# Kernel optimization log

Measured on AMD Instinct MI355X. Metric: run time of the kernel, lower is better.

Reference implementation:

```python
import jax, jax.numpy as jnp
import numpy as np

B, S, D, H, W = 2, 2048, 1024, 16, 256
HD = D // H

def setup_inputs() -> dict:
    key = jax.random.key(0)
    k1, k2, k3 = jax.random.split(key, 3)
    x = jax.random.normal(k1, (B, S, D), dtype=jnp.float32)
    w_qkv = jax.random.normal(k2, (D, 3 * D), dtype=jnp.float32) * (D ** -0.5)
    b_qkv = jnp.zeros((3 * D,), dtype=jnp.float32)
    w_out = jax.random.normal(k3, (D, D), dtype=jnp.float32) * (D ** -0.5)
    b_out = jnp.zeros((D,), dtype=jnp.float32)
    return {"x": x, "w_qkv": w_qkv, "b_qkv": b_qkv, "w_out": w_out, "b_out": b_out}

def reference(x, w_qkv, b_qkv, w_out, b_out):
    b, s, d = x.shape
    qkv = x @ w_qkv + b_qkv                       # [B,S,3D]
    qkv = qkv.reshape(b, s, 3, H, HD)
    q = jnp.transpose(qkv[:, :, 0], (0, 2, 1, 3))  # [B,H,S,HD]
    k = jnp.transpose(qkv[:, :, 1], (0, 2, 1, 3))
    v = jnp.transpose(qkv[:, :, 2], (0, 2, 1, 3))
    # NOTE: original scales by d_model**0.5, not head_dim**0.5
    scores = jnp.einsum('bhqd,bhkd->bhqk', q, k) / (d ** 0.5)
    idx = jnp.arange(s)
    band = jnp.abs(idx[:, None] - idx[None, :]) <= W  # |i-j| <= window_size
    scores = jnp.where(band[None, None], scores, -jnp.inf)
    attn = jax.nn.softmax(scores, axis=-1)
    out = jnp.einsum('bhqk,bhkd->bhqd', attn, v)
    out = jnp.transpose(out, (0, 2, 1, 3)).reshape(b, s, d)
    return out @ w_out + b_out
```

## Files before the change

kernel.cpp:

```cpp
#include <hip/hip_runtime.h>
#include <cstdint>
#include <cmath>

typedef unsigned short u16;
typedef __attribute__((ext_vector_type(8))) short bf16x8;
typedef __attribute__((ext_vector_type(4))) float f32x4;
typedef __attribute__((ext_vector_type(8))) unsigned short u16x8;

#define DEV static __device__ __forceinline__

DEV u16 f2bf(float f) {
  union { float f; uint32_t u; } v; v.f = f;
  uint32_t r = (v.u + 0x7fffu + ((v.u >> 16) & 1u)) >> 16;
  return (u16)r;
}

DEV float fexp2(float x) { return exp2f(x); }

DEV void async16(void* lds, const void* g) {
  __builtin_amdgcn_global_load_lds(
      (const __attribute__((address_space(1))) uint32_t*)g,
      (__attribute__((address_space(3))) uint32_t*)lds, 16, 0, 0);
}

#define QSCALE 0.04508422002778011f

__global__ void conv8(const float* __restrict__ in, u16* __restrict__ out, int n8) {
  int i = blockIdx.x * 256 + threadIdx.x;
  if (i >= n8) return;
  const float4* p = (const float4*)in + (size_t)i * 2;
  float4 a = p[0], b = p[1];
  u16x8 ov;
  ov[0] = f2bf(a.x); ov[1] = f2bf(a.y); ov[2] = f2bf(a.z); ov[3] = f2bf(a.w);
  ov[4] = f2bf(b.x); ov[5] = f2bf(b.y); ov[6] = f2bf(b.z); ov[7] = f2bf(b.w);
  *(u16x8*)(out + (size_t)i * 8) = ov;
}

__global__ void tconv(const float* __restrict__ in, u16* __restrict__ out, int R, int Cdim) {
  __shared__ float t[32][33];
  const int tx = threadIdx.x & 31, ty = threadIdx.x >> 5;
  const int r0 = blockIdx.y * 32, c0 = blockIdx.x * 32;
#pragma unroll
  for (int k = 0; k < 4; ++k) {
    int r = ty + k * 8;
    t[r][tx] = in[(size_t)(r0 + r) * Cdim + c0 + tx];
  }
  __syncthreads();
#pragma unroll
  for (int k = 0; k < 4; ++k) {
    int cc = ty + k * 8;
    out[(size_t)(c0 + cc) * R + r0 + tx] = f2bf(t[tx][cc]);
  }
}

template <int EPI>
__global__ __launch_bounds__(256, 2) void gemm_bt(
    const u16* __restrict__ A, const u16* __restrict__ BT,
    const float* __restrict__ bias, float* __restrict__ C,
    u16* __restrict__ qb, u16* __restrict__ kbuf, u16* __restrict__ vtb,
    int Mdim, int Ndim, int Kdim)
{
  __shared__ u16 Alds[128 * 64];
  __shared__ u16 Blds[128 * 64];
  const int tid = threadIdx.x;
  const int wid = tid >> 6, lane = tid & 63;
  const int g = lane >> 4, c = lane & 15;
  const int wr = wid >> 1, wc = wid & 1;
  const int gx = gridDim.x;
  const int nwg = gx * gridDim.y;
  const int lin = blockIdx.y * gx + blockIdx.x;
  const int work = (lin & 7) * (nwg >> 3) + (lin >> 3);
  const int row0 = (work / gx) * 128, col0 = (work % gx) * 128;

  f32x4 acc[4][4] = {};

  for (int kt = 0; kt < Kdim; kt += 64) {
    __syncthreads();
#pragma unroll
    for (int it = 0; it < 4; ++it) {
      int chunk = wid * 256 + it * 64 + lane;
      int r = chunk >> 3, j = chunk & 7;
      int js = j ^ (r & 7);
      async16((char*)Alds + (wid * 256 + it * 64) * 16,
              A + (size_t)(row0 + r) * Kdim + kt + js * 8);
      async16((char*)Blds + (wid * 256 + it * 64) * 16,
              BT + (size_t)(col0 + r) * Kdim + kt + js * 8);
    }
    __syncthreads();
#pragma unroll
    for (int kk = 0; kk < 2; ++kk) {
      bf16x8 av[4], bv[4];
#pragma unroll
      for (int mi = 0; mi < 4; ++mi) {
        int r = wr * 64 + mi * 16 + c;
        int js = (kk * 4 + g) ^ (r & 7);
        av[mi] = *(const bf16x8*)((const char*)Alds + r * 128 + js * 16);
      }
#pragma unroll
      for (int ni = 0; ni < 4; ++ni) {
        int r = wc * 64 + ni * 16 + c;
        int js = (kk * 4 + g) ^ (r & 7);
        bv[ni] = *(const bf16x8*)((const char*)Blds + r * 128 + js * 16);
      }
#pragma unroll
      for (int mi = 0; mi < 4; ++mi)
#pragma unroll
        for (int ni = 0; ni < 4; ++ni)
          acc[mi][ni] = __builtin_amdgcn_mfma_f32_16x16x32_bf16(
              av[mi], bv[ni], acc[mi][ni], 0, 0, 0);
    }
  }

#pragma unroll
  for (int mi = 0; mi < 4; ++mi) {
#pragma unroll
    for (int ni = 0; ni < 4; ++ni) {
      int colg = col0 + wc * 64 + ni * 16 + c;
      float bsv = bias[colg];
#pragma unroll
      for (int r = 0; r < 4; ++r) {
        int rowg = row0 + wr * 64 + mi * 16 + g * 4 + r;
        float val = acc[mi][ni][r] + bsv;
        if (EPI == 0) {
          C[(size_t)rowg * Ndim + colg] = val;
        } else {
          int t = colg >> 10, rem = colg & 1023;
          int h = rem >> 6, hd = rem & 63;
          int b = rowg >> 11, s = rowg & 2047;
          size_t bho = (size_t)(b * 16 + h);
          if (t == 0)      qb  [(bho * 2048 + s) * 64 + hd] = f2bf(val * QSCALE);
          else if (t == 1) kbuf[(bho * 2048 + s) * 64 + hd] = f2bf(val);
          else             vtb [(bho * 64 + hd) * 2048 + s] = f2bf(val);
        }
      }
    }
  }
}

__global__ __launch_bounds__(512, 4) void attn_win(
    const u16* __restrict__ qb, const u16* __restrict__ kb,
    const u16* __restrict__ vtb, u16* __restrict__ hb)
{
  constexpr int S = 2048, W = 256;
  __shared__ u16 Klds[2][64 * 64];
  __shared__ u16 Vlds[2][64 * 64];
  __shared__ u16 Plds[8][16 * 64];

  const int tid = threadIdx.x, wid = tid >> 6, lane = tid & 63;
  const int g = lane >> 4, c = lane & 15;
  const int lin = blockIdx.x;
  const int work = (lin & 7) * 64 + (lin >> 3);
  const int qt = work & 15, bh = work >> 4;
  const int q0 = qt * 128;
  const int qr0 = q0 + wid * 16;
  const int qw = qr0 + c;
  const size_t bho = (size_t)bh * S * 64;

  bf16x8 aq[2];
  {
    const u16* qrow = qb + bho + (size_t)qw * 64;
    aq[0] = *(const bf16x8*)(qrow + g * 8);
    aq[1] = *(const bf16x8*)(qrow + 32 + g * 8);
  }
  f32x4 o[4] = {};
  float m = -1e30f, lsum = 0.f;

  const int kstart = (q0 - W > 0) ? (q0 - W) : 0;
  const int kend = (q0 + 128 + W < S) ? (q0 + 128 + W) : S;

  const int sr = tid >> 3, sj = tid & 7;
  const int sjs = sj ^ (sr & 7);
#define STAGE(buf, k0s)                                                         \
  {                                                                             \
    async16((char*)&Klds[buf][0] + tid * 16,                                    \
            kb + bho + (size_t)((k0s) + sr) * 64 + sjs * 8);                    \
    async16((char*)&Vlds[buf][0] + tid * 16,                                    \
            vtb + bho + (size_t)sr * S + (k0s) + sjs * 8);                      \
  }

  STAGE(0, kstart);
  asm volatile("s_waitcnt vmcnt(0)" ::: "memory");
  __syncthreads();

  int cur = 0;
  for (int k0 = kstart; k0 < kend; k0 += 64) {
    if (k0 + 64 < kend) STAGE(cur ^ 1, k0 + 64);

    const bool wave_active = !(k0 > qr0 + 15 + W) && !(k0 + 63 < qr0 - W);
    if (wave_active) {
      const u16* Kb = &Klds[cur][0];
      const u16* Vb = &Vlds[cur][0];

      f32x4 sacc[4] = {};
      __builtin_amdgcn_s_setprio(1);
#pragma unroll
      for (int kb4 = 0; kb4 < 4; ++kb4) {
        int krow = kb4 * 16 + c;
#pragma unroll
        for (int kk = 0; kk < 2; ++kk) {
          int js = (kk * 4 + g) ^ (krow & 7);
          bf16x8 bk = *(const bf16x8*)((const char*)Kb + krow * 128 + js * 16);
          sacc[kb4] = __builtin_amdgcn_mfma_f32_16x16x32_bf16(bk, aq[kk], sacc[kb4], 0, 0, 0);
        }
      }
      __builtin_amdgcn_s_setprio(0);

      const bool full = (k0 >= qr0 + 15 - W) && (k0 + 63 <= qr0 + W);
      float sl[4][4];
      if (full) {
#pragma unroll
        for (int kb4 = 0; kb4 < 4; ++kb4)
#pragma unroll
          for (int r = 0; r < 4; ++r) sl[kb4][r] = sacc[kb4][r];
      } else {
#pragma unroll
        for (int kb4 = 0; kb4 < 4; ++kb4) {
#pragma unroll
          for (int r = 0; r < 4; ++r) {
            int key = k0 + kb4 * 16 + g * 4 + r;
            int d = qw - key;
            bool valid = (d <= W) && (d >= -W);
            sl[kb4][r] = valid ? sacc[kb4][r] : -1e30f;
          }
        }
      }

      float mx = fmaxf(
          fmaxf(fmaxf(fmaxf(sl[0][0], sl[0][1]), fmaxf(sl[0][2], sl[0][3])),
                fmaxf(fmaxf(sl[1][0], sl[1][1]), fmaxf(sl[1][2], sl[1][3]))),
          fmaxf(fmaxf(fmaxf(sl[2][0], sl[2][1]), fmaxf(sl[2][2], sl[2][3])),
                fmaxf(fmaxf(sl[3][0], sl[3][1]), fmaxf(sl[3][2], sl[3][3]))));
      mx = fmaxf(mx, __shfl_xor(mx, 16));
      mx = fmaxf(mx, __shfl_xor(mx, 32));

      if (!__all(mx - m <= 8.0f)) {
        float mnew = fmaxf(m, mx);
        float fs = fexp2(m - mnew);
        m = mnew;
        lsum *= fs;
        float fsr[4];
#pragma unroll
        for (int r = 0; r < 4; ++r)
          fsr[r] = __shfl(fs, (lane & 48) | (((lane & 48) >> 2) + r));
#pragma unroll
        for (int nb = 0; nb < 4; ++nb)
#pragma unroll
          for (int r = 0; r < 4; ++r) o[nb][r] *= fsr[r];
      }

      float rsum = 0.f;
      u16* Pw = &Plds[wid][0];
#pragma unroll
      for (int kb4 = 0; kb4 < 4; ++kb4) {
        float p0, p1, p2, p3;
        if (full) {
          p0 = fexp2(sl[kb4][0] - m); p1 = fexp2(sl[kb4][1] - m);
          p2 = fexp2(sl[kb4][2] - m); p3 = fexp2(sl[kb4][3] - m);
        } else {
          p0 = (sl[kb4][0] > -1e29f) ? fexp2(sl[kb4][0] - m) : 0.f;
          p1 = (sl[kb4][1] > -1e29f) ? fexp2(sl[kb4][1] - m) : 0.f;
          p2 = (sl[kb4][2] > -1e29f) ? fexp2(sl[kb4][2] - m) : 0.f;
          p3 = (sl[kb4][3] > -1e29f) ? fexp2(sl[kb4][3] - m) : 0.f;
        }
        rsum += (p0 + p1) + (p2 + p3);
        uint32_t lo, hi;
        asm("v_cvt_pk_bf16_f32 %0, %1, %2" : "=v"(lo) : "v"(p0), "v"(p1));
        asm("v_cvt_pk_bf16_f32 %0, %1, %2" : "=v"(hi) : "v"(p2), "v"(p3));
        uint2 wv; wv.x = lo; wv.y = hi;
        *(uint2*)((char*)Pw + c * 128 + (((kb4 * 2 + (g >> 1)) ^ (c & 7)) << 4) +
                  ((g & 1) << 3)) = wv;
      }
      rsum += __shfl_xor(rsum, 16);
      rsum += __shfl_xor(rsum, 32);
      lsum += rsum;

      asm volatile("s_waitcnt lgkmcnt(0)" ::: "memory");
      __builtin_amdgcn_sched_barrier(0);
      __builtin_amdgcn_s_setprio(1);
#pragma unroll
      for (int ks = 0; ks < 2; ++ks) {
        int js = (ks * 4 + g) ^ (c & 7);
        bf16x8 pa = *(const bf16x8*)((const char*)Pw + c * 128 + js * 16);
#pragma unroll
        for (int nb = 0; nb < 4; ++nb) {
          int hd = nb * 16 + c;
          int vjs = (ks * 4 + g) ^ (hd & 7);
          bf16x8 bv = *(const bf16x8*)((const char*)Vb + hd * 128 + vjs * 16);
          o[nb] = __builtin_amdgcn_mfma_f32_16x16x32_bf16(pa, bv, o[nb], 0, 0, 0);
        }
      }
      __builtin_amdgcn_s_setprio(0);
    }

    asm volatile("s_waitcnt vmcnt(0)" ::: "memory");
    __syncthreads();
    cur ^= 1;
  }
#undef STAGE

  const int b = bh >> 4, h = bh & 15;
  float linv[4];
#pragma unroll
  for (int r = 0; r < 4; ++r)
    linv[r] = 1.0f / __shfl(lsum, (lane & 48) | (((lane & 48) >> 2) + r));
#pragma unroll
  for (int r = 0; r < 4; ++r) {
    int qr = qr0 + g * 4 + r;
#pragma unroll
    for (int nb = 0; nb < 4; ++nb) {
      int col = h * 64 + nb * 16 + c;
      hb[(size_t)(b * 2048 + qr) * 1024 + col] = f2bf(o[nb][r] * linv[r]);
    }
  }
}

extern "C" void kernel_launch(void* const* d_in, const int* in_sizes, int n_in,
                              void* d_out, int out_size, void* d_ws, size_t ws_size,
                              hipStream_t stream) {
  const float* x     = (const float*)d_in[0];
  const float* w_qkv = (const float*)d_in[1];
  const float* b_qkv = (const float*)d_in[2];
  const float* w_out = (const float*)d_in[3];
  const float* b_out = (const float*)d_in[4];
  float* out = (float*)d_out;

  char* ws = (char*)d_ws;
  const size_t MB = 1024 * 1024;
  u16* xbf   = (u16*)(ws);
  u16* wqT   = (u16*)(ws + 8 * MB);
  u16* woT   = (u16*)(ws + 14 * MB);
  u16* qbuf  = (u16*)(ws + 16 * MB);
  u16* kbuf  = (u16*)(ws + 24 * MB);
  u16* vtbuf = (u16*)(ws + 32 * MB);
  u16* hbuf  = (u16*)(ws + 40 * MB);

  conv8<<<dim3(4096 * 1024 / 8 / 256), 256, 0, stream>>>(x, xbf, 4096 * 1024 / 8);
  tconv<<<dim3(3072 / 32, 1024 / 32), 256, 0, stream>>>(w_qkv, wqT, 1024, 3072);
  tconv<<<dim3(1024 / 32, 1024 / 32), 256, 0, stream>>>(w_out, woT, 1024, 1024);
  gemm_bt<1><<<dim3(3072 / 128, 4096 / 128), 256, 0, stream>>>(
      xbf, wqT, b_qkv, nullptr, qbuf, kbuf, vtbuf, 4096, 3072, 1024);
  attn_win<<<dim3(512), 512, 0, stream>>>(qbuf, kbuf, vtbuf, hbuf);
  gemm_bt<0><<<dim3(1024 / 128, 4096 / 128), 256, 0, stream>>>(
      hbuf, woT, b_out, out, nullptr, nullptr, nullptr, 4096, 1024, 1024);
}
```

Before: 169.5 us.

## Add 256x256-tile QKV GEMM kernel with ping-pong LDS pipeline

Swaps the generic 128x128 QKV projection GEMM for a dedicated 256x256-tile kernel with 512 threads. It double-buffers A and B halves in LDS through async global-to-LDS loads, using XOR-swizzled layout and hand-placed waitcnt/barrier/setprio scheduling. The larger tile raises data reuse per byte loaded, and the interleaved staging is meant to overlap memory traffic with MFMA work. The cost is 192 blocks (fewer than the CU count), higher register and LDS pressure, and fragile manual vmcnt accounting.

New measurement: 193.8 us. +14.3%, slower.

```diff
diff --git a/kernel.cpp b/kernel.cpp
--- a/kernel.cpp
+++ b/kernel.cpp
@@ -137,6 +137,150 @@
   }
 }
 
+__global__ __launch_bounds__(512, 2) void gemm256_qkv(
+    const u16* __restrict__ A, const u16* __restrict__ BT,
+    const float* __restrict__ bias,
+    u16* __restrict__ qb, u16* __restrict__ kbuf, u16* __restrict__ vtb)
+{
+  constexpr int K = 1024, NIT = 8;
+  __shared__ u16 lds[2 * 2 * 2 * 8192];
+  const int tid = threadIdx.x;
+  const int lane = tid & 63, wid = tid >> 6;
+  const int g = lane >> 4, c = lane & 15;
+  const int wm = wid >> 2, wn = wid & 3;
+  const int lin = blockIdx.x;
+  const int work = (lin & 7) * 24 + (lin >> 3);
+  const int row0 = (work / 12) * 256, col0 = (work % 12) * 256;
+
+  const int ch0 = tid, ch1 = 512 + tid;
+  const int r0c = ch0 >> 3, j0 = (ch0 & 7) ^ (r0c & 7);
+  const int r1c = ch1 >> 3, j1 = (ch1 & 7) ^ (r1c & 7);
+
+#define STG(ab, buf, half, t)                                                     \
+  {                                                                               \
+    const u16* gp = (ab) ? BT : A;                                                \
+    const int gb = (ab) ? col0 : row0;                                            \
+    u16* lb = lds + (((buf) * 2 + (ab)) * 2 + (half)) * 8192;                     \
+    async16(lb + ch0 * 8, gp + (size_t)(gb + (half) * 128 + r0c) * K + (t) * 64 + j0 * 8); \
+    async16(lb + ch1 * 8, gp + (size_t)(gb + (half) * 128 + r1c) * K + (t) * 64 + j1 * 8); \
+  }
+#define LDA(buf, mh)                                                              \
+  {                                                                               \
+    const u16* rb = lds + (((buf) * 2 + 0) * 2 + (mh)) * 8192;                    \
+    _Pragma("unroll") for (int i = 0; i < 4; ++i) {                               \
+      int rr = wm * 64 + i * 16 + c;                                              \
+      _Pragma("unroll") for (int kk = 0; kk < 2; ++kk)                            \
+        aA[i][kk] = *(const bf16x8*)((const char*)rb + rr * 128 +                 \
+                                     (((kk * 4 + g) ^ (rr & 7)) * 16));           \
+    }                                                                             \
+  }
+#define LDB(buf, nh, dst)                                                         \
+  {                                                                               \
+    const u16* rb = lds + (((buf) * 2 + 1) * 2 + (wn >> 1)) * 8192;               \
+    _Pragma("unroll") for (int j = 0; j < 2; ++j) {                               \
+      int rr = (wn & 1) * 64 + (nh) * 32 + j * 16 + c;                            \
+      _Pragma("unroll") for (int kk = 0; kk < 2; ++kk)                            \
+        dst[j][kk] = *(const bf16x8*)((const char*)rb + rr * 128 +                \
+                                      (((kk * 4 + g) ^ (rr & 7)) * 16));          \
+    }                                                                             \
+  }
+#define MMA(mo, no, bsrc)                                                         \
+  __builtin_amdgcn_s_setprio(1);                                                  \
+  _Pragma("unroll") for (int i = 0; i < 4; ++i)                                   \
+    _Pragma("unroll") for (int j = 0; j < 2; ++j) {                               \
+      acc[(mo) + i][(no) + j] = __builtin_amdgcn_mfma_f32_16x16x32_bf16(          \
+          aA[i][0], bsrc[j][0], acc[(mo) + i][(no) + j], 0, 0, 0);                \
+      acc[(mo) + i][(no) + j] = __builtin_amdgcn_mfma_f32_16x16x32_bf16(          \
+          aA[i][1], bsrc[j][1], acc[(mo) + i][(no) + j], 0, 0, 0);                \
+    }                                                                             \
+  __builtin_amdgcn_s_setprio(0);                                                  \
+  __builtin_amdgcn_sched_barrier(0);
+#define BAR() __builtin_amdgcn_s_barrier()
+
+  f32x4 acc[8][4] = {};
+  bf16x8 aA[4][2], bB0[2][2], bB1[2][2];
+
+  STG(0, 0, 0, 0); STG(1, 0, 0, 0); STG(1, 0, 1, 0); STG(0, 0, 1, 0);
+  STG(0, 1, 0, 1); STG(1, 1, 0, 1); STG(1, 1, 1, 1);
+  asm volatile("s_waitcnt vmcnt(6)" ::: "memory");
+  BAR();
+
+  for (int it = 0; it < NIT; ++it) {
+    const int t1 = 2 * it + 1, t2 = 2 * it + 2, t3 = 2 * it + 3;
+    const bool pf = (it < NIT - 1);
+    LDA(0, 0); LDB(0, 0, bB0);
+    STG(0, 1, 1, t1);
+    BAR();
+    MMA(0, 0, bB0);
+    BAR();
+    LDB(0, 1, bB1);
+    if (pf) STG(0, 0, 0, t2);
+    BAR();
+    MMA(0, 2, bB1);
+    BAR();
+    LDA(0, 1);
+    if (pf) STG(1, 0, 0, t2);
+    BAR();
+    MMA(4, 0, bB0);
+    BAR();
+    if (pf) STG(1, 0, 1, t2);
+    BAR();
+    MMA(4, 2, bB1);
+    if (pf) { asm volatile("s_waitcnt vmcnt(8)" ::: "memory"); }
+    else    { asm volatile("s_waitcnt vmcnt(2)" ::: "memory"); }
+    BAR();
+    LDA(1, 0); LDB(1, 0, bB0);
+    if (pf) STG(0, 0, 1, t2);
+    BAR();
+    MMA(0, 0, bB0);
+    BAR();
+    LDB(1, 1, bB1);
+    if (pf) STG(0, 1, 0, t3);
+    BAR();
+    MMA(0, 2, bB1);
+    if (pf) { asm volatile("s_waitcnt vmcnt(10)" ::: "memory"); }
+    else    { asm volatile("s_waitcnt vmcnt(0)" ::: "memory"); }
+    BAR();
+    LDA(1, 1);
+    if (pf) STG(1, 1, 0, t3);
+    BAR();
+    MMA(4, 0, bB0);
+    BAR();
+    if (pf) STG(1, 1, 1, t3);
+    BAR();
+    MMA(4, 2, bB1);
+    if (pf) { asm volatile("s_waitcnt vmcnt(6)" ::: "memory"); }
+    BAR();
+  }
+#undef STG
+#undef LDA
+#undef LDB
+#undef MMA
+#undef BAR
+
+#pragma unroll
+  for (int MF = 0; MF < 8; ++MF) {
+#pragma unroll
+    for (int NF = 0; NF < 4; ++NF) {
+      int colg = col0 + wn * 64 + NF * 16 + c;
+      float bsv = bias[colg];
+      int rowb = row0 + (MF >> 2) * 128 + wm * 64 + (MF & 3) * 16 + g * 4;
+#pragma unroll
+      for (int r = 0; r < 4; ++r) {
+        int rowg = rowb + r;
+        float val = acc[MF][NF][r] + bsv;
+        int t = colg >> 10, rem = colg & 1023;
+        int h = rem >> 6, hd = rem & 63;
+        int b = rowg >> 11, s = rowg & 2047;
+        size_t bho = (size_t)(b * 16 + h);
+        if (t == 0)      qb  [(bho * 2048 + s) * 64 + hd] = f2bf(val * QSCALE);
+        else if (t == 1) kbuf[(bho * 2048 + s) * 64 + hd] = f2bf(val);
+        else             vtb [(bho * 64 + hd) * 2048 + s] = f2bf(val);
+      }
+    }
+  }
+}
+
 __global__ __launch_bounds__(512, 4) void attn_win(
     const u16* __restrict__ qb, const u16* __restrict__ kb,
     const u16* __restrict__ vtb, u16* __restrict__ hb)
@@ -337,8 +481,7 @@
   conv8<<<dim3(4096 * 1024 / 8 / 256), 256, 0, stream>>>(x, xbf, 4096 * 1024 / 8);
   tconv<<<dim3(3072 / 32, 1024 / 32), 256, 0, stream>>>(w_qkv, wqT, 1024, 3072);
   tconv<<<dim3(1024 / 32, 1024 / 32), 256, 0, stream>>>(w_out, woT, 1024, 1024);
-  gemm_bt<1><<<dim3(3072 / 128, 4096 / 128), 256, 0, stream>>>(
-      xbf, wqT, b_qkv, nullptr, qbuf, kbuf, vtbuf, 4096, 3072, 1024);
+  gemm256_qkv<<<dim3(192), 512, 0, stream>>>(xbf, wqT, b_qkv, qbuf, kbuf, vtbuf);
   attn_win<<<dim3(512), 512, 0, stream>>>(qbuf, kbuf, vtbuf, hbuf);
   gemm_bt<0><<<dim3(1024 / 128, 4096 / 128), 256, 0, stream>>>(
       hbuf, woT, b_out, out, nullptr, nullptr, nullptr, 4096, 1024, 1024);
```

## Triple-buffer K/V tiles in windowed attention and vectorize V-transpose epilogue stores

Applied to the files above, without the earlier changes.

The attention kernel moves from double to triple buffering of K/V LDS tiles. It issues loads two tiles ahead and waits with a partial vmcnt, so each iteration needs one barrier instead of a full drain plus syncthreads. The QKV GEMM epilogue now packs four consecutive sequence positions into one 8-byte store for the transposed V buffer, and folds the Q/K paths into a single loop. LDS use per block grows by two 8KB tiles, which could lower occupancy under the 4-blocks-per-CU launch bound.

Result: faster. 161.9 us (-4.5%).

```diff
diff --git a/kernel.cpp b/kernel.cpp
--- a/kernel.cpp
+++ b/kernel.cpp
@@ -6,6 +6,7 @@
 typedef __attribute__((ext_vector_type(8))) short bf16x8;
 typedef __attribute__((ext_vector_type(4))) float f32x4;
 typedef __attribute__((ext_vector_type(8))) unsigned short u16x8;
+typedef __attribute__((ext_vector_type(4))) unsigned short u16x4;
 
 #define DEV static __device__ __forceinline__
 
@@ -117,20 +118,27 @@
     for (int ni = 0; ni < 4; ++ni) {
       int colg = col0 + wc * 64 + ni * 16 + c;
       float bsv = bias[colg];
-#pragma unroll
-      for (int r = 0; r < 4; ++r) {
-        int rowg = row0 + wr * 64 + mi * 16 + g * 4 + r;
-        float val = acc[mi][ni][r] + bsv;
-        if (EPI == 0) {
-          C[(size_t)rowg * Ndim + colg] = val;
+      int rowb = row0 + wr * 64 + mi * 16 + g * 4;
+      if (EPI == 0) {
+#pragma unroll
+        for (int r = 0; r < 4; ++r)
+          C[(size_t)(rowb + r) * Ndim + colg] = acc[mi][ni][r] + bsv;
+      } else {
+        int t = colg >> 10, rem = colg & 1023;
+        int h = rem >> 6, hd = rem & 63;
+        int b = rowb >> 11, s0 = rowb & 2047;
+        size_t bho = (size_t)(b * 16 + h);
+        if (t == 2) {
+          u16x4 pv;
+#pragma unroll
+          for (int r = 0; r < 4; ++r) pv[r] = f2bf(acc[mi][ni][r] + bsv);
+          *(u16x4*)(vtb + (bho * 64 + hd) * 2048 + s0) = pv;
         } else {
-          int t = colg >> 10, rem = colg & 1023;
-          int h = rem >> 6, hd = rem & 63;
-          int b = rowg >> 11, s = rowg & 2047;
-          size_t bho = (size_t)(b * 16 + h);
-          if (t == 0)      qb  [(bho * 2048 + s) * 64 + hd] = f2bf(val * QSCALE);
-          else if (t == 1) kbuf[(bho * 2048 + s) * 64 + hd] = f2bf(val);
-          else             vtb [(bho * 64 + hd) * 2048 + s] = f2bf(val);
+          u16* dst = (t == 0) ? qb : kbuf;
+          float sc = (t == 0) ? QSCALE : 1.0f;
+#pragma unroll
+          for (int r = 0; r < 4; ++r)
+            dst[(bho * 2048 + (s0 + r)) * 64 + hd] = f2bf((acc[mi][ni][r] + bsv) * sc);
         }
       }
     }
@@ -142,8 +150,8 @@
     const u16* __restrict__ vtb, u16* __restrict__ hb)
 {
   constexpr int S = 2048, W = 256;
-  __shared__ u16 Klds[2][64 * 64];
-  __shared__ u16 Vlds[2][64 * 64];
+  __shared__ u16 Klds[3][64 * 64];
+  __shared__ u16 Vlds[3][64 * 64];
   __shared__ u16 Plds[8][16 * 64];
 
   const int tid = threadIdx.x, wid = tid >> 6, lane = tid & 63;
@@ -167,6 +175,7 @@
 
   const int kstart = (q0 - W > 0) ? (q0 - W) : 0;
   const int kend = (q0 + 128 + W < S) ? (q0 + 128 + W) : S;
+  const int ntiles = (kend - kstart) >> 6;
 
   const int sr = tid >> 3, sj = tid & 7;
   const int sjs = sj ^ (sr & 7);
@@ -179,13 +188,17 @@
   }
 
   STAGE(0, kstart);
-  asm volatile("s_waitcnt vmcnt(0)" ::: "memory");
-  __syncthreads();
-
-  int cur = 0;
-  for (int k0 = kstart; k0 < kend; k0 += 64) {
-    if (k0 + 64 < kend) STAGE(cur ^ 1, k0 + 64);
-
+  if (ntiles > 1) STAGE(1, kstart + 64);
+
+  for (int i = 0; i < ntiles; ++i) {
+    const int k0 = kstart + (i << 6);
+    if (i + 1 < ntiles) { asm volatile("s_waitcnt vmcnt(2)" ::: "memory"); }
+    else                { asm volatile("s_waitcnt vmcnt(0)" ::: "memory"); }
+    __builtin_amdgcn_s_barrier();
+    __builtin_amdgcn_sched_barrier(0);
+    if (i + 2 < ntiles) STAGE((i + 2) % 3, k0 + 128);
+
+    const int cur = i % 3;
     const bool wave_active = !(k0 > qr0 + 15 + W) && !(k0 + 63 < qr0 - W);
     if (wave_active) {
       const u16* Kb = &Klds[cur][0];
@@ -291,10 +304,6 @@
       }
       __builtin_amdgcn_s_setprio(0);
     }
-
-    asm volatile("s_waitcnt vmcnt(0)" ::: "memory");
-    __syncthreads();
-    cur ^= 1;
   }
 #undef STAGE
 
```
